# Optimization experiments

Measured on AMD Instinct MI355X. Metric: run time of the kernel, lower is better.

Reference implementation:

```python
import jax, jax.numpy as jnp
import numpy as np

ALPHA = 0.5
BETA = 0.5
THRESHOLD = 0.5


def _bce_with_logits(x, t):
    # Numerically stable elementwise BCEWithLogitsLoss (reduction='none').
    return jnp.maximum(x, 0.0) - x * t + jnp.log1p(jnp.exp(-jnp.abs(x)))


def _critical_masks(y_pred, y_target, threshold):
    # Proxy for detect_critical: binarize prediction and target, then flag
    # split mistakes (false negatives) and merge mistakes (false positives).
    pred_bin = jax.nn.sigmoid(y_pred) > threshold
    tgt_bin = y_target > 0.5
    neg_mask = jnp.logical_and(tgt_bin, jnp.logical_not(pred_bin)).astype(y_pred.dtype)
    pos_mask = jnp.logical_and(pred_bin, jnp.logical_not(tgt_bin)).astype(y_pred.dtype)
    return neg_mask, pos_mask


def setup_inputs() -> dict:
    key = jax.random.key(0)
    k1, k2 = jax.random.split(key)
    shape = (8, 1, 128, 128, 128)  # [B, C=1, D, H, W]
    y_pred = jax.random.normal(k1, shape, dtype=jnp.float32)
    y_target = jax.random.uniform(k2, shape, dtype=jnp.float32)
    return {"y_pred": y_pred, "y_target": y_target}


def reference(y_pred, y_target):
    neg_mask, pos_mask = _critical_masks(y_pred, y_target, THRESHOLD)
    # Masks come from an external detection routine in the original -> constants.
    neg_mask = jax.lax.stop_gradient(neg_mask)
    pos_mask = jax.lax.stop_gradient(pos_mask)
    loss = _bce_with_logits(y_pred, y_target)
    total = loss * (1.0 + ALPHA * neg_mask + BETA * pos_mask)
    return total.mean()
```

## Files before the change

### kernel.cpp

```cpp
#include <hip/hip_runtime.h>

#define N_TOTAL (8 * 128 * 128 * 128)
#define THREADS 1024
#define BLOCKS  1024
#define STRIDE  (BLOCKS * THREADS)

__device__ __forceinline__ float svl_elem(float x, float t) {
    float loss = fmaxf(x, 0.0f) - x * t + __logf(1.0f + __expf(-fabsf(x)));
    bool pred = x > 0.0f;
    bool tgt  = t > 0.5f;
    float w = (pred != tgt) ? 1.5f : 1.0f;
    return loss * w;
}

__global__ __launch_bounds__(THREADS) void svl_partial_kernel(
        const float* __restrict__ yp, const float* __restrict__ yt,
        float* __restrict__ partial) {
    int idx = blockIdx.x * THREADS + threadIdx.x;

    float acc = 0.0f;
    for (int i = idx; i < N_TOTAL; i += STRIDE)
        acc += svl_elem(yp[i], yt[i]);

    #pragma unroll
    for (int off = 32; off > 0; off >>= 1)
        acc += __shfl_down(acc, off, 64);

    __shared__ float smem[THREADS / 64];
    int lane = threadIdx.x & 63;
    int wave = threadIdx.x >> 6;
    if (lane == 0) smem[wave] = acc;
    __syncthreads();

    if (threadIdx.x == 0) {
        float s = 0.0f;
        #pragma unroll
        for (int w = 0; w < THREADS / 64; ++w) s += smem[w];
        partial[blockIdx.x] = s;
    }
}

__global__ __launch_bounds__(256) void svl_final_kernel(
        const float* __restrict__ partial, float* __restrict__ out) {
    float acc = 0.0f;
    for (int i = threadIdx.x; i < BLOCKS; i += 256)
        acc += partial[i];

    #pragma unroll
    for (int off = 32; off > 0; off >>= 1)
        acc += __shfl_down(acc, off, 64);

    __shared__ float smem[4];
    int lane = threadIdx.x & 63;
    int wave = threadIdx.x >> 6;
    if (lane == 0) smem[wave] = acc;
    __syncthreads();

    if (threadIdx.x == 0) {
        float s = 0.0f;
        #pragma unroll
        for (int w = 0; w < 4; ++w) s += smem[w];
        out[0] = s * (1.0f / (float)N_TOTAL);
    }
}

extern "C" void kernel_launch(void* const* d_in, const int* in_sizes, int n_in,
                              void* d_out, int out_size, void* d_ws, size_t ws_size,
                              hipStream_t stream) {
    const float* yp = (const float*)d_in[0];
    const float* yt = (const float*)d_in[1];
    float* out = (float*)d_out;
    float* partial = (float*)d_ws;

    svl_partial_kernel<<<BLOCKS, THREADS, 0, stream>>>(yp, yt, partial);
    svl_final_kernel<<<1, 256, 0, stream>>>(partial, out);
}
```

Baseline: 142.6 us.

## Stage input tiles into LDS with wide direct global-to-LDS loads

Replaces the grid-stride scalar loads with per-block 4096-element tiles fetched via 16-byte global_load_lds into shared memory, then computes the loss from LDS. Block count rises to 4096 with 256 threads each, and the final reduction uses 1024 threads over the larger partial array. The aim is more bytes in flight per load and better latency hiding. The cost is 32 KB of LDS per block, which limits occupancy, and an extra barrier before compute.

```diff
diff --git a/kernel.cpp b/kernel.cpp
--- a/kernel.cpp
+++ b/kernel.cpp
@@ -1,9 +1,11 @@
 #include <hip/hip_runtime.h>
+#include <stdint.h>
 
 #define N_TOTAL (8 * 128 * 128 * 128)
-#define THREADS 1024
-#define BLOCKS  1024
-#define STRIDE  (BLOCKS * THREADS)
+#define THREADS 256
+#define TILE    4096
+#define BLOCKS  (N_TOTAL / TILE)
+#define FINAL_THREADS 1024
 
 __device__ __forceinline__ float svl_elem(float x, float t) {
     float loss = fmaxf(x, 0.0f) - x * t + __logf(1.0f + __expf(-fabsf(x)));
@@ -16,17 +18,63 @@
 __global__ __launch_bounds__(THREADS) void svl_partial_kernel(
         const float* __restrict__ yp, const float* __restrict__ yt,
         float* __restrict__ partial) {
-    int idx = blockIdx.x * THREADS + threadIdx.x;
+    __shared__ float bp[TILE];
+    __shared__ float bt[TILE];
+
+    const int lane = threadIdx.x & 63;
+    const int wave = threadIdx.x >> 6;
+    const size_t base = (size_t)blockIdx.x * TILE;
+
+    #pragma unroll
+    for (int c = 0; c < 4; ++c) {
+        const int chunk = wave * 4 + c;
+        const int off = chunk * 256 + lane * 4;
+        __builtin_amdgcn_global_load_lds(
+            (const __attribute__((address_space(1))) uint32_t*)(yp + base + off),
+            (__attribute__((address_space(3))) uint32_t*)(bp + chunk * 256),
+            16, 0, 0);
+        __builtin_amdgcn_global_load_lds(
+            (const __attribute__((address_space(1))) uint32_t*)(yt + base + off),
+            (__attribute__((address_space(3))) uint32_t*)(bt + chunk * 256),
+            16, 0, 0);
+    }
+    __syncthreads();
 
     float acc = 0.0f;
-    for (int i = idx; i < N_TOTAL; i += STRIDE)
-        acc += svl_elem(yp[i], yt[i]);
+    #pragma unroll
+    for (int k = 0; k < TILE / THREADS; ++k) {
+        int e = threadIdx.x + k * THREADS;
+        acc += svl_elem(bp[e], bt[e]);
+    }
 
     #pragma unroll
     for (int off = 32; off > 0; off >>= 1)
         acc += __shfl_down(acc, off, 64);
 
-    __shared__ float smem[THREADS / 64];
+    __syncthreads();
+    if (lane == 0) bp[wave] = acc;
+    __syncthreads();
+
+    if (threadIdx.x == 0) {
+        float s = 0.0f;
+        #pragma unroll
+        for (int w = 0; w < THREADS / 64; ++w) s += bp[w];
+        partial[blockIdx.x] = s;
+    }
+}
+
+__global__ __launch_bounds__(FINAL_THREADS) void svl_final_kernel(
+        const float* __restrict__ partial, float* __restrict__ out) {
+    float acc = 0.0f;
+    #pragma unroll
+    for (int i = threadIdx.x; i < BLOCKS; i += FINAL_THREADS)
+        acc += partial[i];
+
+    #pragma unroll
+    for (int off = 32; off > 0; off >>= 1)
+        acc += __shfl_down(acc, off, 64);
+
+    __shared__ float smem[FINAL_THREADS / 64];
     int lane = threadIdx.x & 63;
     int wave = threadIdx.x >> 6;
     if (lane == 0) smem[wave] = acc;
@@ -35,31 +83,7 @@
     if (threadIdx.x == 0) {
         float s = 0.0f;
         #pragma unroll
-        for (int w = 0; w < THREADS / 64; ++w) s += smem[w];
-        partial[blockIdx.x] = s;
-    }
-}
-
-__global__ __launch_bounds__(256) void svl_final_kernel(
-        const float* __restrict__ partial, float* __restrict__ out) {
-    float acc = 0.0f;
-    for (int i = threadIdx.x; i < BLOCKS; i += 256)
-        acc += partial[i];
-
-    #pragma unroll
-    for (int off = 32; off > 0; off >>= 1)
-        acc += __shfl_down(acc, off, 64);
-
-    __shared__ float smem[4];
-    int lane = threadIdx.x & 63;
-    int wave = threadIdx.x >> 6;
-    if (lane == 0) smem[wave] = acc;
-    __syncthreads();
-
-    if (threadIdx.x == 0) {
-        float s = 0.0f;
-        #pragma unroll
-        for (int w = 0; w < 4; ++w) s += smem[w];
+        for (int w = 0; w < FINAL_THREADS / 64; ++w) s += smem[w];
         out[0] = s * (1.0f / (float)N_TOTAL);
     }
 }
@@ -73,5 +97,5 @@
     float* partial = (float*)d_ws;
 
     svl_partial_kernel<<<BLOCKS, THREADS, 0, stream>>>(yp, yt, partial);
-    svl_final_kernel<<<1, 256, 0, stream>>>(partial, out);
+    svl_final_kernel<<<1, FINAL_THREADS, 0, stream>>>(partial, out);
 }
```

Result: no change. 143.6 us (+0.7%).
